# Optimization experiments

Measured on AMD Instinct MI355X. Metric: run time of the kernel, lower is better.

The kernel has to match this reference:

```python
import jax, jax.numpy as jnp
import numpy as np
import math

B, S, D, H = 4, 1024, 1024, 16
DH = D // H  # 64
NEG = -100000000000.0


def setup_inputs() -> dict:
    key = jax.random.key(0)
    ks = jax.random.split(key, 9)
    sc_in = 1.0 / math.sqrt(D)
    sc_h = 1.0 / math.sqrt(DH)
    return {
        "x": jax.random.normal(ks[0], (B, S, D), dtype=jnp.float32),
        # per-head projection weights stacked over the head axis [H, D, DH]
        "Wq": jax.random.normal(ks[1], (H, D, DH), dtype=jnp.float32) * sc_in,
        "bq": jnp.zeros((H, DH), dtype=jnp.float32),
        "Wk": jax.random.normal(ks[2], (H, D, DH), dtype=jnp.float32) * sc_in,
        "bk": jnp.zeros((H, DH), dtype=jnp.float32),
        "Wv": jax.random.normal(ks[3], (H, D, DH), dtype=jnp.float32) * sc_in,
        "bv": jnp.zeros((H, DH), dtype=jnp.float32),
        # output feed-forward: Dense(D, gelu) applied to the [B,S,DH] head-sum
        "Wf": jax.random.normal(ks[4], (DH, D), dtype=jnp.float32) * sc_h,
        "bf": jnp.zeros((D,), dtype=jnp.float32),
    }


def reference(x, Wq, bq, Wk, bk, Wv, bv, Wf, bf):
    # per-head q,k,v: [B,H,S,DH]
    q = jnp.einsum('bsd,hde->bhse', x, Wq) + bq[None, :, None, :]
    k = jnp.einsum('bsd,hde->bhse', x, Wk) + bk[None, :, None, :]
    v = jnp.einsum('bsd,hde->bhse', x, Wv) + bv[None, :, None, :]
    scale = 1.0 / math.sqrt(DH)
    # causal mask as in source: triu(ones, 1) * -1e11 added to scores
    mask = jnp.triu(jnp.ones((S, S), dtype=jnp.float32), 1) * NEG
    scores = jnp.einsum('bhse,bhte->bhst', q, k) * scale + mask  # [B,H,S,S]
    w = jax.nn.softmax(scores, axis=-1)
    z = jnp.einsum('bhst,bhte->bhse', w, v)  # [B,H,S,DH]
    # faithful to source bug: heads are SUMMED, not concatenated
    summed = jnp.sum(z, axis=1)  # [B,S,DH]
    # ff Dense with exact (erf) gelu, keras tf.nn.gelu default approximate=False
    out = jax.nn.gelu(summed @ Wf + bf, approximate=False)  # [B,S,D]
    # dropout is identity at inference
    return out
```

## Files before the change

### kernel.cpp

```cpp
#include <hip/hip_runtime.h>
#include <hip/hip_bf16.h>
#include <math.h>

#define BB 4
#define SS 1024
#define DD 1024
#define HH 16
#define DH 64

#define GM 4096
#define GN 3072
#define GK 1024

typedef __attribute__((ext_vector_type(4))) float f32x4;
typedef __attribute__((ext_vector_type(8))) short bf16x8;

__device__ __forceinline__ unsigned int pack2bf(float a, float b) {
    __hip_bfloat16 x = __float2bfloat16(a), y = __float2bfloat16(b);
    return (unsigned int)__builtin_bit_cast(unsigned short, x) |
           ((unsigned int)__builtin_bit_cast(unsigned short, y) << 16);
}

__device__ __forceinline__ int swz8(int row) { return (row ^ (row >> 2)) & 7; }

__global__ __launch_bounds__(256) void convert_x(const float* __restrict__ x,
                                                 __hip_bfloat16* __restrict__ xb)
{
    int i = (blockIdx.x * 256 + threadIdx.x) * 4;
    float4 xv = *(const float4*)(x + i);
    xb[i + 0] = __float2bfloat16(xv.x);
    xb[i + 1] = __float2bfloat16(xv.y);
    xb[i + 2] = __float2bfloat16(xv.z);
    xb[i + 3] = __float2bfloat16(xv.w);
}

__global__ __launch_bounds__(256) void wt_kernel(
    const float* __restrict__ Wq, const float* __restrict__ Wk,
    const float* __restrict__ Wv, __hip_bfloat16* __restrict__ WbT)
{
    const int z = blockIdx.y >> 4;
    const int h = blockIdx.y & 15;
    const int d0 = blockIdx.x * 64;
    const int tid = threadIdx.x;
    const float* W = (z == 0) ? Wq : (z == 1) ? Wk : Wv;
    const float* src = W + (size_t)h * DD * DH;

    __shared__ float tile[64][65];

    #pragma unroll
    for (int p = 0; p < 16; p++) {
        int d = p * 4 + (tid >> 6);
        int e = tid & 63;
        tile[d][e] = src[(size_t)(d0 + d) * DH + e];
    }
    __syncthreads();
    #pragma unroll
    for (int p = 0; p < 16; p++) {
        int e = p * 4 + (tid >> 6);
        int d = tid & 63;
        WbT[(size_t)(z * 1024 + h * 64 + e) * GK + d0 + d] =
            __float2bfloat16(tile[d][e]);
    }
}

__global__ __launch_bounds__(256) void wft_kernel(
    const float* __restrict__ Wf, unsigned short* __restrict__ WfT)
{
    const int d0 = blockIdx.x * 64;
    const int tid = threadIdx.x;
    __shared__ float tile[64][65];

    #pragma unroll
    for (int p = 0; p < 16; p++) {
        int e  = p * 4 + (tid >> 6);
        int dd = tid & 63;
        tile[e][dd] = Wf[(size_t)e * DD + d0 + dd];
    }
    __syncthreads();
    #pragma unroll
    for (int p = 0; p < 16; p++) {
        int dd = p * 4 + (tid >> 6);
        int e  = tid & 63;
        __hip_bfloat16 hb = __float2bfloat16(tile[e][dd]);
        WfT[(size_t)(d0 + dd) * DH + e] =
            __builtin_bit_cast(unsigned short, hb);
    }
}

__global__ __launch_bounds__(256) void gemm_qkv(
    const unsigned short* __restrict__ A,
    const unsigned short* __restrict__ Bt,
    const float* __restrict__ bq, const float* __restrict__ bk,
    const float* __restrict__ bv,
    unsigned short* __restrict__ q, unsigned short* __restrict__ k,
    unsigned short* __restrict__ v)
{
    __shared__ unsigned short As[128 * 64];
    __shared__ unsigned short Bs[128 * 64];

    const int tid  = threadIdx.x;
    const int wave = tid >> 6;
    const int lane = tid & 63;
    const int m0 = blockIdx.x * 128;
    const int n0 = blockIdx.y * 128;
    const int wy = wave >> 1, wx = wave & 1;
    const bool vblk = (n0 >= 2048);

    f32x4 acc[4][4];
    #pragma unroll
    for (int i = 0; i < 4; i++)
        #pragma unroll
        for (int j = 0; j < 4; j++)
            acc[i][j] = (f32x4){0.f, 0.f, 0.f, 0.f};

    const int srow0 = (wave * 4) * 8;
    const int lrow  = lane >> 3;
    const int lcs   = lane & 7;

    for (int ko = 0; ko < GK; ko += 64) {
        __syncthreads();
        #pragma unroll
        for (int c = 0; c < 4; c++) {
            int row = srow0 + c * 8 + lrow;
            int chunk = lcs ^ (row & 7);
            const unsigned short* ga = A + (size_t)(m0 + row) * GK + ko + chunk * 8;
            const unsigned short* gb = Bt + (size_t)(n0 + row) * GK + ko + chunk * 8;
            unsigned short* la = As + ((size_t)(wave * 4 + c) * 64) * 8;
            unsigned short* lb = Bs + ((size_t)(wave * 4 + c) * 64) * 8;
            __builtin_amdgcn_global_load_lds(
                (const __attribute__((address_space(1))) unsigned int*)ga,
                (__attribute__((address_space(3))) unsigned int*)la, 16, 0, 0);
            __builtin_amdgcn_global_load_lds(
                (const __attribute__((address_space(1))) unsigned int*)gb,
                (__attribute__((address_space(3))) unsigned int*)lb, 16, 0, 0);
        }
        __syncthreads();

        const int mrow = lane & 15;
        const int quad = lane >> 4;
        #pragma unroll
        for (int ks = 0; ks < 2; ks++) {
            bf16x8 af[4], bfr[4];
            #pragma unroll
            for (int mt = 0; mt < 4; mt++) {
                int row = wy * 64 + mt * 16 + mrow;
                int chunk = (ks * 4 + quad) ^ (row & 7);
                af[mt] = *(const bf16x8*)(As + row * 64 + chunk * 8);
            }
            #pragma unroll
            for (int nt = 0; nt < 4; nt++) {
                int row = wx * 64 + nt * 16 + mrow;
                int chunk = (ks * 4 + quad) ^ (row & 7);
                bfr[nt] = *(const bf16x8*)(Bs + row * 64 + chunk * 8);
            }
            if (vblk) {
                #pragma unroll
                for (int mt = 0; mt < 4; mt++)
                    #pragma unroll
                    for (int nt = 0; nt < 4; nt++)
                        acc[mt][nt] = __builtin_amdgcn_mfma_f32_16x16x32_bf16(
                            af[mt], bfr[nt], acc[mt][nt], 0, 0, 0);
            } else {
                #pragma unroll
                for (int nt = 0; nt < 4; nt++)
                    #pragma unroll
                    for (int mt = 0; mt < 4; mt++)
                        acc[nt][mt] = __builtin_amdgcn_mfma_f32_16x16x32_bf16(
                            bfr[nt], af[mt], acc[nt][mt], 0, 0, 0);
            }
        }
    }

    const int quad = lane >> 4;
    const int cl   = lane & 15;
    const int h    = ((n0 + wx * 64) >> 6) & 15;

    if (!vblk) {
        const int z = n0 >> 10;
        const float* bias = (z == 0) ? bq : bk;
        unsigned short* outp = (z == 0) ? q : k;
        const float sc = (z == 0) ? 0.125f : 1.0f;
        #pragma unroll
        for (int nt = 0; nt < 4; nt++) {
            int ebase = nt * 16 + quad * 4;
            float4 b4 = *(const float4*)(bias + h * 64 + ebase);
            #pragma unroll
            for (int mt = 0; mt < 4; mt++) {
                int m = m0 + wy * 64 + mt * 16 + cl;
                int b = m >> 10, s = m & 1023;
                f32x4 a = acc[nt][mt];
                float v0 = (a[0] + b4.x) * sc;
                float v1 = (a[1] + b4.y) * sc;
                float v2 = (a[2] + b4.z) * sc;
                float v3 = (a[3] + b4.w) * sc;
                uint2 pk = make_uint2(pack2bf(v0, v1), pack2bf(v2, v3));
                *(uint2*)(outp + ((size_t)((b * 16 + h) * 1024 + s)) * 64 + ebase) = pk;
            }
        }
    } else {
        #pragma unroll
        for (int nt = 0; nt < 4; nt++) {
            int e = nt * 16 + cl;
            float bb = bv[h * 64 + e];
            #pragma unroll
            for (int mt = 0; mt < 4; mt++) {
                int rbase = m0 + wy * 64 + mt * 16 + quad * 4;
                int b = rbase >> 10, s = rbase & 1023;
                f32x4 a = acc[mt][nt];
                uint2 pk = make_uint2(pack2bf(a[0] + bb, a[1] + bb),
                                      pack2bf(a[2] + bb, a[3] + bb));
                *(uint2*)(v + ((size_t)((b * 16 + h) * 64 + e)) * 1024 + s) = pk;
            }
        }
    }
}

__global__ __launch_bounds__(256) void flash_attn(
    const unsigned short* __restrict__ qg, const unsigned short* __restrict__ kg,
    const unsigned short* __restrict__ vtg, float* __restrict__ summed)
{
    __shared__ unsigned short Qs[4096];
    __shared__ unsigned short Ks[2][4096];
    __shared__ unsigned short Vts[2][4096];

    const int x  = blockIdx.x;
    const int y  = blockIdx.y;
    const int qi = (x + (y & 15) + ((y >> 4) << 2)) & 15;
    const int q0 = qi * 64;
    const int bh = y;
    const int b  = bh >> 4;
    const int tid  = threadIdx.x;
    const int wave = tid >> 6;
    const int lane = tid & 63;
    const int lrow = lane >> 3;
    const int lcs  = lane & 7;
    const int m16  = lane & 15;
    const int quad = lane >> 4;

    const unsigned short* qb = qg + (size_t)bh * SS * DH;
    const unsigned short* kb = kg + (size_t)bh * SS * DH;
    const unsigned short* vb = vtg + (size_t)bh * SS * DH;

    #pragma unroll
    for (int c = 0; c < 2; c++) {
        int region = wave * 2 + c;
        int row = region * 8 + lrow;
        int g = lcs ^ swz8(row);
        __builtin_amdgcn_global_load_lds(
            (const __attribute__((address_space(1))) unsigned int*)
                (qb + (size_t)(q0 + row) * DH + g * 8),
            (__attribute__((address_space(3))) unsigned int*)(Qs + region * 512),
            16, 0, 0);
        __builtin_amdgcn_global_load_lds(
            (const __attribute__((address_space(1))) unsigned int*)
                (kb + (size_t)row * DH + g * 8),
            (__attribute__((address_space(3))) unsigned int*)(&Ks[0][region * 512]),
            16, 0, 0);
        __builtin_amdgcn_global_load_lds(
            (const __attribute__((address_space(1))) unsigned int*)
                (vb + (size_t)row * SS + g * 8),
            (__attribute__((address_space(3))) unsigned int*)(&Vts[0][region * 512]),
            16, 0, 0);
    }

    f32x4 accO[4];
    float lsum = 0.f;
    #pragma unroll
    for (int nt = 0; nt < 4; nt++) accO[nt] = (f32x4){0.f, 0.f, 0.f, 0.f};

    bf16x8 af0, af1;
    const int rloc = wave * 16 + m16;

    for (int tt = 0; tt <= qi; tt++) {
        __syncthreads();

        if (tt == 0) {
            int row = wave * 16 + m16;
            af0 = *(const bf16x8*)(Qs + row * 64 + ((quad ^ swz8(row)) * 8));
            af1 = *(const bf16x8*)(Qs + row * 64 + (((4 + quad) ^ swz8(row)) * 8));
        }

        if (tt < qi) {
            const int t1 = (tt + 1) * 64;
            const int bn = (tt + 1) & 1;
            #pragma unroll
            for (int c = 0; c < 2; c++) {
                int region = wave * 2 + c;
                int row = region * 8 + lrow;
                int g = lcs ^ swz8(row);
                __builtin_amdgcn_global_load_lds(
                    (const __attribute__((address_space(1))) unsigned int*)
                        (kb + (size_t)(t1 + row) * DH + g * 8),
                    (__attribute__((address_space(3))) unsigned int*)
                        (&Ks[bn][region * 512]), 16, 0, 0);
                __builtin_amdgcn_global_load_lds(
                    (const __attribute__((address_space(1))) unsigned int*)
                        (vb + (size_t)row * SS + t1 + g * 8),
                    (__attribute__((address_space(3))) unsigned int*)
                        (&Vts[bn][region * 512]), 16, 0, 0);
            }
        }

        const unsigned short* uK = &Ks[tt & 1][0];
        const unsigned short* uV = &Vts[tt & 1][0];

        f32x4 acc[4];
        #pragma unroll
        for (int nt = 0; nt < 4; nt++) {
            int row = ((nt & 2) << 4) + ((m16 >> 2) << 3) + ((nt & 1) << 2) + (m16 & 3);
            bf16x8 kf0 = *(const bf16x8*)(uK + row * 64 + ((quad ^ swz8(row)) * 8));
            bf16x8 kf1 = *(const bf16x8*)(uK + row * 64 + (((4 + quad) ^ swz8(row)) * 8));
            f32x4 a = (f32x4){0.f, 0.f, 0.f, 0.f};
            a = __builtin_amdgcn_mfma_f32_16x16x32_bf16(kf0, af0, a, 0, 0, 0);
            a = __builtin_amdgcn_mfma_f32_16x16x32_bf16(kf1, af1, a, 0, 0, 0);
            acc[nt] = a;
        }

        const bool diag = (tt == qi);
        bf16x8 pf0, pf1;
        #pragma unroll
        for (int nt = 0; nt < 4; nt++) {
            #pragma unroll
            for (int r = 0; r < 4; r++) {
                int tl = ((nt & 2) << 4) + (quad << 3) + ((nt & 1) << 2) + r;
                float s = acc[nt][r];
                if (diag && tl > rloc) s = -1e30f;
                float p = __expf(s);
                lsum += p;
                __hip_bfloat16 hb = __float2bfloat16(p);
                short pb = (short)__builtin_bit_cast(unsigned short, hb);
                int j = ((nt & 1) << 2) + r;
                if (nt < 2) pf0[j] = pb; else pf1[j] = pb;
            }
        }

        #pragma unroll
        for (int nt = 0; nt < 4; nt++) {
            int row = nt * 16 + m16;
            bf16x8 vf0 = *(const bf16x8*)(uV + row * 64 + ((quad ^ swz8(row)) * 8));
            bf16x8 vf1 = *(const bf16x8*)(uV + row * 64 + (((4 + quad) ^ swz8(row)) * 8));
            accO[nt] = __builtin_amdgcn_mfma_f32_16x16x32_bf16(vf0, pf0, accO[nt],
                                                               0, 0, 0);
            accO[nt] = __builtin_amdgcn_mfma_f32_16x16x32_bf16(vf1, pf1, accO[nt],
                                                               0, 0, 0);
        }
    }

    float l = lsum;
    l += __shfl_xor(l, 16);
    l += __shfl_xor(l, 32);
    const float invl = 1.f / l;

    __syncthreads();
    float* buf = (wave < 2) ? (float*)&Ks[0][0] : (float*)&Vts[0][0];
    buf += (wave & 1) * (16 * 66);
    #pragma unroll
    for (int nt = 0; nt < 4; nt++) {
        f32x4 w4 = accO[nt];
        w4 *= invl;
        *(f32x4*)(buf + m16 * 66 + nt * 16 + quad * 4) = w4;
    }
    __asm__ volatile("s_waitcnt lgkmcnt(0)" ::: "memory");

    float* dstbase = summed + ((size_t)b * SS + q0 + wave * 16) * DH;
    #pragma unroll
    for (int rr = 0; rr < 16; rr++) {
        float valr = buf[rr * 66 + lane];
        atomicAdd(dstbase + (size_t)rr * DH + lane, valr);
    }
}

__global__ __launch_bounds__(256) void ff_mfma(
    const float* __restrict__ summed, const unsigned short* __restrict__ WfT,
    const float* __restrict__ bfb, float* __restrict__ out)
{
    __shared__ unsigned short As[128 * 64];
    __shared__ unsigned short Bs[128 * 64];

    const int tid  = threadIdx.x;
    const int wave = tid >> 6;
    const int lane = tid & 63;
    const int m0 = blockIdx.x * 128;
    const int n0 = blockIdx.y * 128;
    const int wy = wave >> 1, wx = wave & 1;
    const int lrow = lane >> 3;
    const int lcs  = lane & 7;

    #pragma unroll
    for (int c = 0; c < 4; c++) {
        int row = (wave * 4 + c) * 8 + lrow;
        int chunk = lcs ^ (row & 7);
        __builtin_amdgcn_global_load_lds(
            (const __attribute__((address_space(1))) unsigned int*)
                (WfT + (size_t)(n0 + row) * DH + chunk * 8),
            (__attribute__((address_space(3))) unsigned int*)
                (Bs + ((wave * 4 + c) * 64) * 8), 16, 0, 0);
    }
    #pragma unroll
    for (int i = 0; i < 4; i++) {
        int chunkid = tid + i * 256;
        int row = chunkid >> 3, c = chunkid & 7;
        const float* src = summed + (size_t)(m0 + row) * DH + c * 8;
        float4 a = *(const float4*)src;
        float4 bq = *(const float4*)(src + 4);
        uint4 pk;
        pk.x = pack2bf(a.x, a.y);  pk.y = pack2bf(a.z, a.w);
        pk.z = pack2bf(bq.x, bq.y); pk.w = pack2bf(bq.z, bq.w);
        *(uint4*)(As + row * 64 + ((c ^ (row & 7)) * 8)) = pk;
    }
    __syncthreads();

    f32x4 acc[4][4];
    #pragma unroll
    for (int i = 0; i < 4; i++)
        #pragma unroll
        for (int j = 0; j < 4; j++)
            acc[i][j] = (f32x4){0.f, 0.f, 0.f, 0.f};

    const int mrow = lane & 15;
    const int quad = lane >> 4;
    #pragma unroll
    for (int ks = 0; ks < 2; ks++) {
        bf16x8 af[4], bfr[4];
        #pragma unroll
        for (int mt = 0; mt < 4; mt++) {
            int row = wy * 64 + mt * 16 + mrow;
            int chunk = (ks * 4 + quad) ^ (row & 7);
            af[mt] = *(const bf16x8*)(As + row * 64 + chunk * 8);
        }
        #pragma unroll
        for (int nt = 0; nt < 4; nt++) {
            int row = wx * 64 + nt * 16 + mrow;
            int chunk = (ks * 4 + quad) ^ (row & 7);
            bfr[nt] = *(const bf16x8*)(Bs + row * 64 + chunk * 8);
        }
        #pragma unroll
        for (int mt = 0; mt < 4; mt++)
            #pragma unroll
            for (int nt = 0; nt < 4; nt++)
                acc[mt][nt] = __builtin_amdgcn_mfma_f32_16x16x32_bf16(
                    af[mt], bfr[nt], acc[mt][nt], 0, 0, 0);
    }

    const int cl = lane & 15;
    #pragma unroll
    for (int nt = 0; nt < 4; nt++) {
        int d = n0 + wx * 64 + nt * 16 + cl;
        float bb = bfb[d];
        #pragma unroll
        for (int mt = 0; mt < 4; mt++) {
            int rbase = m0 + wy * 64 + mt * 16 + quad * 4;
            #pragma unroll
            for (int r = 0; r < 4; r++) {
                float vA = acc[mt][nt][r] + bb;
                out[(size_t)(rbase + r) * DD + d] =
                    0.5f * vA * (1.f + erff(vA * 0.70710678118654752f));
            }
        }
    }
}

extern "C" void kernel_launch(void* const* d_in, const int* in_sizes, int n_in,
                              void* d_out, int out_size, void* d_ws, size_t ws_size,
                              hipStream_t stream) {
    const float* x  = (const float*)d_in[0];
    const float* Wq = (const float*)d_in[1];
    const float* bq = (const float*)d_in[2];
    const float* Wk = (const float*)d_in[3];
    const float* bk = (const float*)d_in[4];
    const float* Wv = (const float*)d_in[5];
    const float* bv = (const float*)d_in[6];
    const float* Wf = (const float*)d_in[7];
    const float* bf = (const float*)d_in[8];
    float* out = (float*)d_out;

    const size_t per = (size_t)BB * HH * SS * DH;
    unsigned short* q   = (unsigned short*)d_ws;
    unsigned short* k   = q + per;
    unsigned short* v   = k + per;
    float* summed       = (float*)(v + per);
    __hip_bfloat16* xb  = (__hip_bfloat16*)(summed + (size_t)BB * SS * DH);
    __hip_bfloat16* WbT = xb + (size_t)BB * SS * DD;
    unsigned short* WfT = (unsigned short*)(WbT + (size_t)GN * GK);

    hipMemsetAsync(summed, 0, (size_t)BB * SS * DH * sizeof(float), stream);

    convert_x<<<(BB * SS * DD) / (256 * 4), 256, 0, stream>>>(x, xb);
    wt_kernel<<<dim3(DD / 64, 3 * HH), 256, 0, stream>>>(Wq, Wk, Wv, WbT);
    wft_kernel<<<DD / 64, 256, 0, stream>>>(Wf, WfT);

    gemm_qkv<<<dim3(GM / 128, GN / 128), 256, 0, stream>>>(
        (const unsigned short*)xb, (const unsigned short*)WbT,
        bq, bk, bv, q, k, v);

    flash_attn<<<dim3(SS / 64, BB * HH), 256, 0, stream>>>(q, k, v, summed);

    ff_mfma<<<dim3(GM / 128, DD / 128), 256, 0, stream>>>(summed, WfT, bf, out);
}
```

Before: 173.9 us.

## Double-buffer QKV GEMM LDS tiles and merge prep kernels into one launch

```diff
diff --git a/kernel.cpp b/kernel.cpp
--- a/kernel.cpp
+++ b/kernel.cpp
@@ -23,67 +23,62 @@
 
 __device__ __forceinline__ int swz8(int row) { return (row ^ (row >> 2)) & 7; }
 
-__global__ __launch_bounds__(256) void convert_x(const float* __restrict__ x,
-                                                 __hip_bfloat16* __restrict__ xb)
-{
-    int i = (blockIdx.x * 256 + threadIdx.x) * 4;
-    float4 xv = *(const float4*)(x + i);
-    xb[i + 0] = __float2bfloat16(xv.x);
-    xb[i + 1] = __float2bfloat16(xv.y);
-    xb[i + 2] = __float2bfloat16(xv.z);
-    xb[i + 3] = __float2bfloat16(xv.w);
-}
-
-__global__ __launch_bounds__(256) void wt_kernel(
+__global__ __launch_bounds__(256) void prep_kernel(
+    const float* __restrict__ x, __hip_bfloat16* __restrict__ xb,
     const float* __restrict__ Wq, const float* __restrict__ Wk,
-    const float* __restrict__ Wv, __hip_bfloat16* __restrict__ WbT)
-{
-    const int z = blockIdx.y >> 4;
-    const int h = blockIdx.y & 15;
-    const int d0 = blockIdx.x * 64;
-    const int tid = threadIdx.x;
-    const float* W = (z == 0) ? Wq : (z == 1) ? Wk : Wv;
-    const float* src = W + (size_t)h * DD * DH;
-
-    __shared__ float tile[64][65];
-
-    #pragma unroll
-    for (int p = 0; p < 16; p++) {
-        int d = p * 4 + (tid >> 6);
-        int e = tid & 63;
-        tile[d][e] = src[(size_t)(d0 + d) * DH + e];
-    }
-    __syncthreads();
-    #pragma unroll
-    for (int p = 0; p < 16; p++) {
-        int e = p * 4 + (tid >> 6);
-        int d = tid & 63;
-        WbT[(size_t)(z * 1024 + h * 64 + e) * GK + d0 + d] =
-            __float2bfloat16(tile[d][e]);
-    }
-}
-
-__global__ __launch_bounds__(256) void wft_kernel(
+    const float* __restrict__ Wv, __hip_bfloat16* __restrict__ WbT,
     const float* __restrict__ Wf, unsigned short* __restrict__ WfT)
 {
-    const int d0 = blockIdx.x * 64;
+    const int id  = blockIdx.x;
     const int tid = threadIdx.x;
     __shared__ float tile[64][65];
 
-    #pragma unroll
-    for (int p = 0; p < 16; p++) {
-        int e  = p * 4 + (tid >> 6);
-        int dd = tid & 63;
-        tile[e][dd] = Wf[(size_t)e * DD + d0 + dd];
-    }
-    __syncthreads();
-    #pragma unroll
-    for (int p = 0; p < 16; p++) {
-        int dd = p * 4 + (tid >> 6);
-        int e  = tid & 63;
-        __hip_bfloat16 hb = __float2bfloat16(tile[e][dd]);
-        WfT[(size_t)(d0 + dd) * DH + e] =
-            __builtin_bit_cast(unsigned short, hb);
+    if (id < 4096) {
+        int i = (id * 256 + tid) * 4;
+        float4 xv = *(const float4*)(x + i);
+        xb[i + 0] = __float2bfloat16(xv.x);
+        xb[i + 1] = __float2bfloat16(xv.y);
+        xb[i + 2] = __float2bfloat16(xv.z);
+        xb[i + 3] = __float2bfloat16(xv.w);
+    } else if (id < 4864) {
+        const int idx = id - 4096;
+        const int d0  = (idx & 15) * 64;
+        const int zh  = idx >> 4;
+        const int z   = zh >> 4;
+        const int h   = zh & 15;
+        const float* W = (z == 0) ? Wq : (z == 1) ? Wk : Wv;
+        const float* src = W + (size_t)h * DD * DH;
+        #pragma unroll
+        for (int p = 0; p < 16; p++) {
+            int d = p * 4 + (tid >> 6);
+            int e = tid & 63;
+            tile[d][e] = src[(size_t)(d0 + d) * DH + e];
+        }
+        __syncthreads();
+        #pragma unroll
+        for (int p = 0; p < 16; p++) {
+            int e = p * 4 + (tid >> 6);
+            int d = tid & 63;
+            WbT[(size_t)(z * 1024 + h * 64 + e) * GK + d0 + d] =
+                __float2bfloat16(tile[d][e]);
+        }
+    } else {
+        const int d0 = (id - 4864) * 64;
+        #pragma unroll
+        for (int p = 0; p < 16; p++) {
+            int e  = p * 4 + (tid >> 6);
+            int dd = tid & 63;
+            tile[e][dd] = Wf[(size_t)e * DD + d0 + dd];
+        }
+        __syncthreads();
+        #pragma unroll
+        for (int p = 0; p < 16; p++) {
+            int dd = p * 4 + (tid >> 6);
+            int e  = tid & 63;
+            __hip_bfloat16 hb = __float2bfloat16(tile[e][dd]);
+            WfT[(size_t)(d0 + dd) * DH + e] =
+                __builtin_bit_cast(unsigned short, hb);
+        }
     }
 }
 
@@ -95,8 +90,8 @@
     unsigned short* __restrict__ q, unsigned short* __restrict__ k,
     unsigned short* __restrict__ v)
 {
-    __shared__ unsigned short As[128 * 64];
-    __shared__ unsigned short Bs[128 * 64];
+    __shared__ unsigned short As[2][128 * 32];
+    __shared__ unsigned short Bs[2][128 * 32];
 
     const int tid  = threadIdx.x;
     const int wave = tid >> 6;
@@ -113,67 +108,77 @@
         for (int j = 0; j < 4; j++)
             acc[i][j] = (f32x4){0.f, 0.f, 0.f, 0.f};
 
-    const int srow0 = (wave * 4) * 8;
-    const int lrow  = lane >> 3;
-    const int lcs   = lane & 7;
-
-    for (int ko = 0; ko < GK; ko += 64) {
+    const int lrow2 = lane >> 2;
+    const int lslot = lane & 3;
+    const int kchsw = lslot ^ ((lrow2 >> 1) & 3);
+
+    #define STAGE(bufidx, ki)                                                  \
+        {                                                                      \
+            int k0 = (ki) * 32;                                                \
+            _Pragma("unroll")                                                  \
+            for (int c = 0; c < 2; c++) {                                      \
+                int region = wave * 2 + c;                                     \
+                int row = region * 16 + lrow2;                                 \
+                const unsigned short* ga =                                     \
+                    A + (size_t)(m0 + row) * GK + k0 + kchsw * 8;              \
+                const unsigned short* gb =                                     \
+                    Bt + (size_t)(n0 + row) * GK + k0 + kchsw * 8;             \
+                __builtin_amdgcn_global_load_lds(                              \
+                    (const __attribute__((address_space(1))) unsigned int*)ga, \
+                    (__attribute__((address_space(3))) unsigned int*)          \
+                        (&As[bufidx][region * 512]), 16, 0, 0);                \
+                __builtin_amdgcn_global_load_lds(                              \
+                    (const __attribute__((address_space(1))) unsigned int*)gb, \
+                    (__attribute__((address_space(3))) unsigned int*)          \
+                        (&Bs[bufidx][region * 512]), 16, 0, 0);                \
+            }                                                                  \
+        }
+
+    STAGE(0, 0);
+
+    const int mrow = lane & 15;
+    const int quad = lane >> 4;
+
+    for (int ki = 0; ki < 32; ki++) {
         __syncthreads();
-        #pragma unroll
-        for (int c = 0; c < 4; c++) {
-            int row = srow0 + c * 8 + lrow;
-            int chunk = lcs ^ (row & 7);
-            const unsigned short* ga = A + (size_t)(m0 + row) * GK + ko + chunk * 8;
-            const unsigned short* gb = Bt + (size_t)(n0 + row) * GK + ko + chunk * 8;
-            unsigned short* la = As + ((size_t)(wave * 4 + c) * 64) * 8;
-            unsigned short* lb = Bs + ((size_t)(wave * 4 + c) * 64) * 8;
-            __builtin_amdgcn_global_load_lds(
-                (const __attribute__((address_space(1))) unsigned int*)ga,
-                (__attribute__((address_space(3))) unsigned int*)la, 16, 0, 0);
-            __builtin_amdgcn_global_load_lds(
-                (const __attribute__((address_space(1))) unsigned int*)gb,
-                (__attribute__((address_space(3))) unsigned int*)lb, 16, 0, 0);
-        }
-        __syncthreads();
-
-        const int mrow = lane & 15;
-        const int quad = lane >> 4;
-        #pragma unroll
-        for (int ks = 0; ks < 2; ks++) {
-            bf16x8 af[4], bfr[4];
-            #pragma unroll
-            for (int mt = 0; mt < 4; mt++) {
-                int row = wy * 64 + mt * 16 + mrow;
-                int chunk = (ks * 4 + quad) ^ (row & 7);
-                af[mt] = *(const bf16x8*)(As + row * 64 + chunk * 8);
-            }
-            #pragma unroll
-            for (int nt = 0; nt < 4; nt++) {
-                int row = wx * 64 + nt * 16 + mrow;
-                int chunk = (ks * 4 + quad) ^ (row & 7);
-                bfr[nt] = *(const bf16x8*)(Bs + row * 64 + chunk * 8);
-            }
-            if (vblk) {
+        if (ki < 31) STAGE((ki + 1) & 1, ki + 1);
+
+        const unsigned short* uA = &As[ki & 1][0];
+        const unsigned short* uB = &Bs[ki & 1][0];
+
+        bf16x8 af[4], bfr[4];
+        #pragma unroll
+        for (int mt = 0; mt < 4; mt++) {
+            int row = wy * 64 + mt * 16 + mrow;
+            int chunk = quad ^ ((row >> 1) & 3);
+            af[mt] = *(const bf16x8*)(uA + row * 32 + chunk * 8);
+        }
+        #pragma unroll
+        for (int nt = 0; nt < 4; nt++) {
+            int row = wx * 64 + nt * 16 + mrow;
+            int chunk = quad ^ ((row >> 1) & 3);
+            bfr[nt] = *(const bf16x8*)(uB + row * 32 + chunk * 8);
+        }
+        if (vblk) {
+            #pragma unroll
+            for (int mt = 0; mt < 4; mt++)
+                #pragma unroll
+                for (int nt = 0; nt < 4; nt++)
+                    acc[mt][nt] = __builtin_amdgcn_mfma_f32_16x16x32_bf16(
+                        af[mt], bfr[nt], acc[mt][nt], 0, 0, 0);
+        } else {
+            #pragma unroll
+            for (int nt = 0; nt < 4; nt++)
                 #pragma unroll
                 for (int mt = 0; mt < 4; mt++)
-                    #pragma unroll
-                    for (int nt = 0; nt < 4; nt++)
-                        acc[mt][nt] = __builtin_amdgcn_mfma_f32_16x16x32_bf16(
-                            af[mt], bfr[nt], acc[mt][nt], 0, 0, 0);
-            } else {
-                #pragma unroll
-                for (int nt = 0; nt < 4; nt++)
-                    #pragma unroll
-                    for (int mt = 0; mt < 4; mt++)
-                        acc[nt][mt] = __builtin_amdgcn_mfma_f32_16x16x32_bf16(
-                            bfr[nt], af[mt], acc[nt][mt], 0, 0, 0);
-            }
-        }
-    }
-
-    const int quad = lane >> 4;
-    const int cl   = lane & 15;
-    const int h    = ((n0 + wx * 64) >> 6) & 15;
+                    acc[nt][mt] = __builtin_amdgcn_mfma_f32_16x16x32_bf16(
+                        bfr[nt], af[mt], acc[nt][mt], 0, 0, 0);
+        }
+    }
+    #undef STAGE
+
+    const int cl = lane & 15;
+    const int h  = ((n0 + wx * 64) >> 6) & 15;
 
     if (!vblk) {
         const int z = n0 >> 10;
@@ -485,9 +490,9 @@
 
     hipMemsetAsync(summed, 0, (size_t)BB * SS * DH * sizeof(float), stream);
 
-    convert_x<<<(BB * SS * DD) / (256 * 4), 256, 0, stream>>>(x, xb);
-    wt_kernel<<<dim3(DD / 64, 3 * HH), 256, 0, stream>>>(Wq, Wk, Wv, WbT);
-    wft_kernel<<<DD / 64, 256, 0, stream>>>(Wf, WfT);
+    prep_kernel<<<4880, 256, 0, stream>>>(x, (__hip_bfloat16*)xb,
+                                          Wq, Wk, Wv, (__hip_bfloat16*)WbT,
+                                          Wf, WfT);
 
     gemm_qkv<<<dim3(GM / 128, GN / 128), 256, 0, stream>>>(
         (const unsigned short*)xb, (const unsigned short*)WbT,
```

Result: slower. 182.5 us (+4.9%).
